# Optimization experiments

Hardware: AMD Instinct MI355X
Metric: run time of the kernel (lower is better)

The kernel has to match this reference:

```python
import jax, jax.numpy as jnp
import numpy as np
from jax import lax

N_REF = 500000   # reference cohort size
N_PC = 128       # PCA components
N_FEAT = 2000    # raw feature dim
TOP_K = 16


def setup_inputs() -> dict:
    key = jax.random.key(0)
    k1, k2, k3, k4 = jax.random.split(key, 4)
    data_in = jax.random.normal(k1, (1, N_FEAT), dtype=jnp.float32)
    transform_mat = jax.random.normal(k2, (N_FEAT, N_PC), dtype=jnp.float32)
    ref_data = jax.random.normal(k3, (N_REF, N_PC), dtype=jnp.float32)
    psuedo = jax.random.uniform(k4, (N_REF,), dtype=jnp.float32)
    return {
        "data_in": data_in,
        "transform_mat": transform_mat,
        "ref_data": ref_data,
        "psuedo": psuedo,
        "K": TOP_K,
    }


def reference(data_in, transform_mat, ref_data, psuedo, K):
    # project query into PCA space: [1, P]
    data_in_pc = jnp.matmul(data_in, transform_mat)
    # L1 distance to every reference sample: [N]
    dist = jnp.sum(jnp.abs(data_in_pc - ref_data), axis=1)
    # K nearest neighbors (smallest distances); ties irrelevant for mean
    _, top_k_ind = lax.top_k(-dist, K)
    inference_score = jnp.mean(psuedo[top_k_ind])
    return inference_score[None]  # shape [1], matches tf.expand_dims
```

## Files before the change

### kernel.cpp

```cpp
#include <hip/hip_runtime.h>
#include <stdint.h>

#define N_REF   500000
#define N_PC    128
#define N_FEAT  2000
#define TOPK    16

#define K1_BLOCKS  2048
#define K1_THREADS 256
#define K1_WAVES   (K1_BLOCKS * (K1_THREADS / 64))
#define N_PAIRS    (N_REF / 2)
#define NCAND      (K1_BLOCKS * TOPK)

typedef unsigned long long u64;

__device__ __forceinline__ void insert16(u64* top, u64 x) {
#pragma unroll
    for (int i = 15; i >= 1; --i) {
        u64 lo = top[i - 1];
        u64 hi = (x > lo) ? x : lo;
        top[i] = (top[i] < hi) ? top[i] : hi;
    }
    top[0] = (top[0] < x) ? top[0] : x;
}

__device__ __forceinline__ u64 bitonic_sort64(u64 v, int lane) {
#pragma unroll
    for (int k = 2; k <= 64; k <<= 1) {
#pragma unroll
        for (int j = k >> 1; j >= 1; j >>= 1) {
            u64 o = __shfl_xor(v, j);
            bool up    = ((lane & k) == 0);
            bool lower = ((lane & j) == 0);
            u64 mn = (v < o) ? v : o;
            u64 mx = (v < o) ? o : v;
            v = (up == lower) ? mn : mx;
        }
    }
    return v;
}

__global__ void proj_partial(const float* __restrict__ din,
                             const float* __restrict__ T,
                             float* __restrict__ part) {
    int b = blockIdx.x;
    int t = threadIdx.x;
    int f0 = b * 125;
    float acc = 0.f;
#pragma unroll 5
    for (int f = f0; f < f0 + 125; ++f)
        acc += din[f] * T[(size_t)f * 128 + t];
    part[b * 128 + t] = acc;
}

__global__ __launch_bounds__(K1_THREADS) void dist_topk(
        const float* __restrict__ part,
        const float* __restrict__ ref,
        u64* __restrict__ cand) {
    __shared__ __align__(16) float pc[N_PC];
    __shared__ u64 wl[64];

    int tid  = threadIdx.x;
    int lane = tid & 63;
    int w    = tid >> 6;

    if (tid < N_PC) {
        float s = 0.f;
#pragma unroll
        for (int b = 0; b < 16; ++b) s += part[b * N_PC + tid];
        pc[tid] = s;
    }
    __syncthreads();

    float4 qv = reinterpret_cast<const float4*>(pc)[lane & 31];

    u64 top[TOPK];
#pragma unroll
    for (int i = 0; i < TOPK; ++i) top[i] = ~0ull;

    int gw = blockIdx.x * (K1_THREADS / 64) + w;
    const float4* ref4 = reinterpret_cast<const float4*>(ref);

    for (int pair = gw; pair < N_PAIRS; pair += K1_WAVES) {
        float4 v = ref4[(size_t)pair * 64 + lane];
        float d = fabsf(qv.x - v.x) + fabsf(qv.y - v.y)
                + fabsf(qv.z - v.z) + fabsf(qv.w - v.w);
#pragma unroll
        for (int off = 16; off >= 1; off >>= 1)
            d += __shfl_xor(d, off);
        unsigned b0 = (unsigned)__builtin_amdgcn_readlane(__float_as_int(d), 0);
        unsigned b1 = (unsigned)__builtin_amdgcn_readlane(__float_as_int(d), 32);
        u64 k0 = (((u64)b0) << 32) | (u64)(2u * (unsigned)pair);
        u64 k1 = (((u64)b1) << 32) | (u64)(2u * (unsigned)pair + 1u);
        if (k0 < top[TOPK - 1]) insert16(top, k0);
        if (k1 < top[TOPK - 1]) insert16(top, k1);
    }

    if (lane == 0) {
#pragma unroll
        for (int i = 0; i < TOPK; ++i) wl[w * TOPK + i] = top[i];
    }
    __syncthreads();

    if (tid < 64) {
        u64 v = bitonic_sort64(wl[tid], tid);
        if (tid < TOPK) cand[blockIdx.x * TOPK + tid] = v;
    }
}

__global__ __launch_bounds__(256) void final_topk(
        const u64* __restrict__ cand,
        const float* __restrict__ psuedo,
        float* __restrict__ out) {
    __shared__ u64 wl[64];
    int tid  = threadIdx.x;
    int lane = tid & 63;
    int w    = tid >> 6;

    u64 top[TOPK];
#pragma unroll
    for (int i = 0; i < TOPK; ++i) top[i] = ~0ull;

    for (int i = tid; i < NCAND; i += 256) {
        u64 x = cand[i];
        if (x < top[TOPK - 1]) insert16(top, x);
    }

    u64 chosen = 0;
#pragma unroll
    for (int r = 0; r < TOPK; ++r) {
        u64 m = top[0];
#pragma unroll
        for (int off = 32; off >= 1; off >>= 1) {
            u64 o = __shfl_xor(m, off);
            m = (o < m) ? o : m;
        }
        if (top[0] == m) {
#pragma unroll
            for (int i = 0; i < TOPK - 1; ++i) top[i] = top[i + 1];
            top[TOPK - 1] = ~0ull;
        }
        if (lane == r) chosen = m;
    }
    if (lane < TOPK) wl[w * TOPK + lane] = chosen;
    __syncthreads();

    if (tid < 64) {
        u64 v = bitonic_sort64(wl[tid], tid);
        float p = 0.f;
        if (tid < TOPK) p = psuedo[(unsigned)(v & 0xffffffffull)];
#pragma unroll
        for (int off = 32; off >= 1; off >>= 1)
            p += __shfl_xor(p, off);
        if (tid == 0) out[0] = p * (1.0f / (float)TOPK);
    }
}

extern "C" void kernel_launch(void* const* d_in, const int* in_sizes, int n_in,
                              void* d_out, int out_size, void* d_ws, size_t ws_size,
                              hipStream_t stream) {
    const float* din = (const float*)d_in[0];
    const float* T   = (const float*)d_in[1];
    const float* ref = (const float*)d_in[2];
    const float* ps  = (const float*)d_in[3];

    float* part = (float*)d_ws;
    u64*   cand = (u64*)((char*)d_ws + 8192);
    float* outp = (float*)d_out;

    proj_partial<<<16, 128, 0, stream>>>(din, T, part);
    dist_topk<<<K1_BLOCKS, K1_THREADS, 0, stream>>>(part, ref, cand);
    final_topk<<<1, 256, 0, stream>>>(cand, ps, outp);
}
```

Baseline: 465.8 us.

## Split distance computation and top-k into separate kernels via a distance buffer

The fused distance+top-k kernel is split in two. The first kernel streams the reference rows, handling four rows per wave iteration, and writes raw L1 distances to a workspace buffer. A second kernel runs a thread-parallel top-16 over those distances and keeps the existing wave-reduction merge. This removes the serial per-wave insertion bottleneck, where every lane of a wave redundantly maintained the same list. The cost is a 2 MB round trip to memory and an extra launch; the projection is also spread over more blocks.

```diff
diff --git a/kernel.cpp b/kernel.cpp
--- a/kernel.cpp
+++ b/kernel.cpp
@@ -9,8 +9,13 @@
 #define K1_BLOCKS  2048
 #define K1_THREADS 256
 #define K1_WAVES   (K1_BLOCKS * (K1_THREADS / 64))
-#define N_PAIRS    (N_REF / 2)
-#define NCAND      (K1_BLOCKS * TOPK)
+#define N_QUAD     (N_REF / 4)
+
+#define PROJ_BLOCKS 40
+#define FEAT_PER_BLK 50
+
+#define K2_BLOCKS  128
+#define NCAND      (K2_BLOCKS * TOPK)
 
 typedef unsigned long long u64;
 
@@ -45,20 +50,21 @@
                              float* __restrict__ part) {
     int b = blockIdx.x;
     int t = threadIdx.x;
-    int f0 = b * 125;
+    int f0 = b * FEAT_PER_BLK;
     float acc = 0.f;
-#pragma unroll 5
-    for (int f = f0; f < f0 + 125; ++f)
-        acc += din[f] * T[(size_t)f * 128 + t];
-    part[b * 128 + t] = acc;
-}
-
-__global__ __launch_bounds__(K1_THREADS) void dist_topk(
+#pragma unroll 10
+    for (int i = 0; i < FEAT_PER_BLK; ++i) {
+        int f = f0 + i;
+        acc += din[f] * T[(size_t)f * N_PC + t];
+    }
+    part[b * N_PC + t] = acc;
+}
+
+__global__ __launch_bounds__(K1_THREADS) void dist_stream(
         const float* __restrict__ part,
         const float* __restrict__ ref,
-        u64* __restrict__ cand) {
+        float* __restrict__ dist) {
     __shared__ __align__(16) float pc[N_PC];
-    __shared__ u64 wl[64];
 
     int tid  = threadIdx.x;
     int lane = tid & 63;
@@ -67,39 +73,71 @@
     if (tid < N_PC) {
         float s = 0.f;
 #pragma unroll
-        for (int b = 0; b < 16; ++b) s += part[b * N_PC + tid];
+        for (int b = 0; b < PROJ_BLOCKS; ++b) s += part[b * N_PC + tid];
         pc[tid] = s;
     }
     __syncthreads();
 
     float4 qv = reinterpret_cast<const float4*>(pc)[lane & 31];
-
-    u64 top[TOPK];
-#pragma unroll
-    for (int i = 0; i < TOPK; ++i) top[i] = ~0ull;
 
     int gw = blockIdx.x * (K1_THREADS / 64) + w;
     const float4* ref4 = reinterpret_cast<const float4*>(ref);
 
-    for (int pair = gw; pair < N_PAIRS; pair += K1_WAVES) {
-        float4 v = ref4[(size_t)pair * 64 + lane];
-        float d = fabsf(qv.x - v.x) + fabsf(qv.y - v.y)
-                + fabsf(qv.z - v.z) + fabsf(qv.w - v.w);
-#pragma unroll
-        for (int off = 16; off >= 1; off >>= 1)
-            d += __shfl_xor(d, off);
-        unsigned b0 = (unsigned)__builtin_amdgcn_readlane(__float_as_int(d), 0);
-        unsigned b1 = (unsigned)__builtin_amdgcn_readlane(__float_as_int(d), 32);
-        u64 k0 = (((u64)b0) << 32) | (u64)(2u * (unsigned)pair);
-        u64 k1 = (((u64)b1) << 32) | (u64)(2u * (unsigned)pair + 1u);
-        if (k0 < top[TOPK - 1]) insert16(top, k0);
-        if (k1 < top[TOPK - 1]) insert16(top, k1);
-    }
-
-    if (lane == 0) {
-#pragma unroll
-        for (int i = 0; i < TOPK; ++i) wl[w * TOPK + i] = top[i];
-    }
+    for (int g = gw; g < N_QUAD; g += K1_WAVES) {
+        size_t base = (size_t)g * 128;
+        float4 va = ref4[base + lane];
+        float4 vb = ref4[base + 64 + lane];
+        float d0 = fabsf(qv.x - va.x) + fabsf(qv.y - va.y)
+                 + fabsf(qv.z - va.z) + fabsf(qv.w - va.w);
+        float d1 = fabsf(qv.x - vb.x) + fabsf(qv.y - vb.y)
+                 + fabsf(qv.z - vb.z) + fabsf(qv.w - vb.w);
+#pragma unroll
+        for (int off = 16; off >= 1; off >>= 1) {
+            d0 += __shfl_xor(d0, off);
+            d1 += __shfl_xor(d1, off);
+        }
+        if ((lane & 31) == 0) {
+            int half = lane >> 5;
+            dist[4 * g + half]     = d0;
+            dist[4 * g + 2 + half] = d1;
+        }
+    }
+}
+
+__global__ __launch_bounds__(256) void topk_dist(
+        const float* __restrict__ dist,
+        u64* __restrict__ cand) {
+    __shared__ u64 wl[64];
+    int tid  = threadIdx.x;
+    int lane = tid & 63;
+    int w    = tid >> 6;
+
+    u64 top[TOPK];
+#pragma unroll
+    for (int i = 0; i < TOPK; ++i) top[i] = ~0ull;
+
+    for (int i = blockIdx.x * 256 + tid; i < N_REF; i += K2_BLOCKS * 256) {
+        u64 key = (((u64)(unsigned)__float_as_int(dist[i])) << 32) | (unsigned)i;
+        if (key < top[TOPK - 1]) insert16(top, key);
+    }
+
+    u64 chosen = 0;
+#pragma unroll
+    for (int r = 0; r < TOPK; ++r) {
+        u64 m = top[0];
+#pragma unroll
+        for (int off = 32; off >= 1; off >>= 1) {
+            u64 o = __shfl_xor(m, off);
+            m = (o < m) ? o : m;
+        }
+        if (top[0] == m) {
+#pragma unroll
+            for (int i = 0; i < TOPK - 1; ++i) top[i] = top[i + 1];
+            top[TOPK - 1] = ~0ull;
+        }
+        if (lane == r) chosen = m;
+    }
+    if (lane < TOPK) wl[w * TOPK + lane] = chosen;
     __syncthreads();
 
     if (tid < 64) {
@@ -165,10 +203,12 @@
     const float* ps  = (const float*)d_in[3];
 
     float* part = (float*)d_ws;
-    u64*   cand = (u64*)((char*)d_ws + 8192);
+    float* dist = (float*)((char*)d_ws + 32768);
+    u64*   cand = (u64*)((char*)d_ws + 32768 + N_REF * 4);
     float* outp = (float*)d_out;
 
-    proj_partial<<<16, 128, 0, stream>>>(din, T, part);
-    dist_topk<<<K1_BLOCKS, K1_THREADS, 0, stream>>>(part, ref, cand);
+    proj_partial<<<PROJ_BLOCKS, 128, 0, stream>>>(din, T, part);
+    dist_stream<<<K1_BLOCKS, K1_THREADS, 0, stream>>>(part, ref, dist);
+    topk_dist<<<K2_BLOCKS, 256, 0, stream>>>(dist, cand);
     final_topk<<<1, 256, 0, stream>>>(cand, ps, outp);
 }
```

After: 394.1 us. -15.4%, faster.
